# Optimization experiments

Hardware: AMD Instinct MI355X
Metric: run time of the kernel (lower is better)

The kernel has to match this reference:

```python
import jax, jax.numpy as jnp
import numpy as np

TOP_K = 2
TEMP = 1.0  # router_temperature


def setup_inputs() -> dict:
    key = jax.random.key(0)
    ks = jax.random.split(key, 6)
    B, L, D, F, E, DT = 32, 2048, 512, 1024, 8, 16
    x = jax.random.normal(ks[0], (B, L, D), dtype=jnp.float32)
    z_task = jax.random.normal(ks[1], (B, DT), dtype=jnp.float32)
    tau = jnp.ones((B, 1), dtype=jnp.float32)
    Wr = jax.random.normal(ks[2], (D + DT, E), dtype=jnp.float32) * 0.02
    br = jnp.zeros((E,), dtype=jnp.float32)
    W1 = jax.random.normal(ks[3], (E, D, F), dtype=jnp.float32) * 0.02
    b1 = jnp.zeros((E, F), dtype=jnp.float32)
    W2 = jax.random.normal(ks[4], (E, F, D), dtype=jnp.float32) * 0.02
    b2 = jnp.zeros((E, D), dtype=jnp.float32)
    return dict(x=x, z_task=z_task, tau=tau, Wr=Wr, br=br, W1=W1, b1=b1, W2=W2, b2=b2)


def reference(x, z_task, tau, Wr, br, W1, b1, W2, b2):
    """TaskAdaptiveMoE forward: task-conditioned top-k router + expert dispatch/combine.

    x: [B, L, D], z_task: [B, d_task], tau: [B, 1]. Returns (y [B,L,D], aux_loss scalar).
    """
    B, L, D = x.shape
    E = Wr.shape[1]
    # Router fusion mode 'concat': concat token features with broadcast task token.
    z = jnp.broadcast_to(z_task[:, None, :], (B, L, z_task.shape[-1]))
    router_in = jnp.concatenate([x, z], axis=-1)            # [B, L, D+DT]
    logits = router_in @ Wr + br                             # [B, L, E]
    logits = logits / (TEMP * tau[:, :, None])               # temperature + per-sample tau

    # Top-k gating: softmax over the selected logits only.
    top_vals, top_idx = jax.lax.top_k(logits, TOP_K)         # [B, L, k]
    gates = jax.nn.softmax(top_vals, axis=-1)                # [B, L, k]
    onehot = jax.nn.one_hot(top_idx, E, dtype=x.dtype)       # [B, L, k, E]
    dense_gates = jnp.einsum('blk,blke->ble', gates, onehot)  # [B, L, E], sparse (top-k) combine weights

    # Dispatch/combine: loop over the small fixed expert set to bound memory.
    y = jnp.zeros_like(x)
    for e in range(E):
        h = jax.nn.gelu(x @ W1[e] + b1[e], approximate=False)  # [B, L, F]
        y = y + dense_gates[..., e:e + 1] * (h @ W2[e] + b2[e])

    # Load-balancing auxiliary loss: E * sum(load_fraction * mean_router_prob).
    probs = jax.nn.softmax(logits, axis=-1)                  # [B, L, E]
    importance = probs.mean(axis=(0, 1))                     # [E]
    load = onehot.sum(axis=2).mean(axis=(0, 1))              # [E] fraction of tokens hitting expert
    aux_loss = E * jnp.sum(load * importance)
    return y, aux_loss
```

## Files before the change

kernel.cpp:

```cpp
#include <hip/hip_runtime.h>
#include <hip/hip_bf16.h>
#include <math.h>

typedef _Float16 f16;
typedef __attribute__((ext_vector_type(8))) _Float16 f16x8;
typedef __attribute__((ext_vector_type(4))) float f32x4;

#define TOKENS 65536
#define D_ 512
#define F_ 1024
#define E_ 8
#define DT_ 16
#define TEMP_ 1.0f
#define RANKBIT (1 << 30)

#define OFF_CNT   0
#define OFF_IMP   64
#define OFF_TOK   4096
#define OFF_GATE  (OFF_TOK  + E_*TOKENS*4)
#define OFF_W1P   (OFF_GATE + E_*TOKENS*4)
#define OFF_W2P   (OFF_W1P  + E_*F_*D_*2)
#define OFF_REC1  (OFF_W2P  + E_*F_*D_*2)
#define REC1_BYTES ((size_t)TOKENS * D_ * 2)
#define WS_NEED   ((size_t)OFF_REC1 + REC1_BYTES)

__global__ __launch_bounds__(256) void k_pack(const float* __restrict__ src,
                                              f16* __restrict__ dst, int R, int C)
{
  __shared__ float tile[128][17];
  int e = blockIdx.z, ct = blockIdx.y, kp = blockIdx.x;
  const float* s = src + (size_t)e * R * C + (size_t)(kp * 128) * C + ct * 16;
  int t = threadIdx.x;
  int c = t & 15, r0 = t >> 4;
  #pragma unroll
  for (int p = 0; p < 8; ++p)
    tile[r0 + p * 16][c] = s[(size_t)(r0 + p * 16) * C + c];
  __syncthreads();
  int ksl = t >> 6, l = t & 63, l15 = l & 15, lq = l >> 4;
  f16x8 v;
  #pragma unroll
  for (int j = 0; j < 8; ++j) v[j] = (f16)tile[ksl * 32 + lq * 8 + j][l15];
  f16* d = dst + ((((size_t)e * (C / 16) + ct) * (R / 32)) + kp * 4 + ksl) * 512 + l * 8;
  *(f16x8*)d = v;
}

__global__ __launch_bounds__(256) void k_router(
    const float* __restrict__ x, const float* __restrict__ z, const float* __restrict__ tau,
    const float* __restrict__ Wr, const float* __restrict__ br,
    int* __restrict__ gcnt, float* __restrict__ gimp,
    int* __restrict__ tokrec, float* __restrict__ gaterec)
{
  __shared__ float zlog[E_];
  __shared__ float stau;
  __shared__ int   recI[128];
  __shared__ float rg0[128], rg1[128];
  __shared__ int   pos0[128], pos1[128];
  __shared__ int   lcnt[E_], lbase[E_];
  __shared__ float limp[E_];

  int tid = threadIdx.x, lane = tid & 63, w = tid >> 6;
  int t0 = blockIdx.x * 128;
  int b = t0 >> 11;

  if (tid < E_) {
    float s = br[tid];
    #pragma unroll
    for (int dt = 0; dt < DT_; ++dt) s += z[b * DT_ + dt] * Wr[(D_ + dt) * E_ + tid];
    zlog[tid] = s;
    lcnt[tid] = 0; limp[tid] = 0.f;
  }
  if (tid == 0) stau = TEMP_ * tau[b];

  float wreg[8][8];
  const float* wp = Wr + lane * 64;
  #pragma unroll
  for (int j = 0; j < 8; ++j) {
    f32x4 a = *(const f32x4*)(wp + j * 8);
    f32x4 c = *(const f32x4*)(wp + j * 8 + 4);
    wreg[j][0]=a[0]; wreg[j][1]=a[1]; wreg[j][2]=a[2]; wreg[j][3]=a[3];
    wreg[j][4]=c[0]; wreg[j][5]=c[1]; wreg[j][6]=c[2]; wreg[j][7]=c[3];
  }
  __syncthreads();
  float tv = stau;
  float imp[E_];
  #pragma unroll
  for (int e2 = 0; e2 < E_; ++e2) imp[e2] = 0.f;

  for (int i = 0; i < 32; ++i) {
    int li = w * 32 + i;
    int t = t0 + li;
    const float* xr = x + (size_t)t * D_ + lane * 8;
    f32x4 xa = *(const f32x4*)xr;
    f32x4 xb = *(const f32x4*)(xr + 4);
    float v[E_];
    #pragma unroll
    for (int e2 = 0; e2 < E_; ++e2)
      v[e2] = xa[0]*wreg[0][e2] + xa[1]*wreg[1][e2] + xa[2]*wreg[2][e2] + xa[3]*wreg[3][e2]
            + xb[0]*wreg[4][e2] + xb[1]*wreg[5][e2] + xb[2]*wreg[6][e2] + xb[3]*wreg[7][e2];
    #pragma unroll
    for (int s = 0; s < 6; ++s) {
      #pragma unroll
      for (int e2 = 0; e2 < E_; ++e2) v[e2] += __shfl_xor(v[e2], 1 << s, 64);
    }
    if (lane == 0) {
      #pragma unroll
      for (int e2 = 0; e2 < E_; ++e2) v[e2] = (v[e2] + zlog[e2]) / tv;
      int i0 = 0; float b0v = v[0];
      #pragma unroll
      for (int e2 = 1; e2 < E_; ++e2) if (v[e2] > b0v) { b0v = v[e2]; i0 = e2; }
      int i1 = -1; float b1v = -3.4e38f;
      #pragma unroll
      for (int e2 = 0; e2 < E_; ++e2) if (e2 != i0 && v[e2] > b1v) { b1v = v[e2]; i1 = e2; }
      float ee = expf(b1v - b0v);
      float g0 = 1.f / (1.f + ee);
      recI[li] = i0 | (i1 << 4);
      rg0[li] = g0; rg1[li] = ee * g0;
      float ssum = 0.f, pe[E_];
      #pragma unroll
      for (int e2 = 0; e2 < E_; ++e2) { pe[e2] = expf(v[e2] - b0v); ssum += pe[e2]; }
      float inv = 1.f / ssum;
      #pragma unroll
      for (int e2 = 0; e2 < E_; ++e2) imp[e2] += pe[e2] * inv;
    }
  }
  if (lane == 0) {
    #pragma unroll
    for (int e2 = 0; e2 < E_; ++e2) atomicAdd(&limp[e2], imp[e2]);
  }
  __syncthreads();
  if (tid < 128) {
    int r = recI[tid], i0 = r & 15, i1 = r >> 4;
    pos0[tid] = atomicAdd(&lcnt[i0], 1);
    pos1[tid] = atomicAdd(&lcnt[i1], 1);
  }
  __syncthreads();
  if (tid < E_) {
    lbase[tid] = atomicAdd(&gcnt[tid], lcnt[tid]);
    atomicAdd(&gimp[tid], limp[tid]);
  }
  __syncthreads();
  if (tid < 128) {
    int r = recI[tid], i0 = r & 15, i1 = r >> 4;
    int t = t0 + tid;
    int o0 = i0 * TOKENS + lbase[i0] + pos0[tid];
    int o1 = i1 * TOKENS + lbase[i1] + pos1[tid];
    tokrec[o0] = t;            gaterec[o0] = rg0[tid];
    tokrec[o1] = t | RANKBIT;  gaterec[o1] = rg1[tid];
  }
}

__device__ __forceinline__ float gelu_f(float v)
{
  float u = v * 0.70710678118654752f;
  float au = fabsf(u);
  float t = __builtin_amdgcn_rcpf(1.f + 0.3275911f * au);
  float p = t * (0.254829592f + t * (-0.284496736f + t * (1.421413741f +
            t * (-1.453152027f + t * 1.061405429f))));
  float er = 1.f - p * __expf(-u * u);
  return 0.5f * v * (1.f + copysignf(er, v));
}

__global__ __launch_bounds__(1024, 4) void k_mlp(
    const float* __restrict__ x,
    const f16* __restrict__ W1p, const float* __restrict__ b1,
    const f16* __restrict__ W2p, const float* __restrict__ b2,
    const int* __restrict__ gcnt, const int* __restrict__ tokrec,
    const float* __restrict__ gaterec,
    f16* __restrict__ rec1, float* __restrict__ y, int use_rec)
{
  int e    = blockIdx.x & 7;
  int tile = blockIdx.x >> 3;
  int cnt  = gcnt[e];
  int start = tile * 128;
  if (start >= cnt) return;

  __shared__ f16   xs[128 * 512];
  __shared__ f16   hs[128 * 64];
  __shared__ int   stok[128];
  __shared__ float sgate[128];

  int tid = threadIdx.x, lane = tid & 63, w = tid >> 6;
  int l15 = lane & 15, lq = lane >> 4, lk8 = lq * 8;

  const int*   tokE  = tokrec  + e * TOKENS;
  const float* gateE = gaterec + e * TOKENS;

  if (tid < 128) {
    int idx = start + tid;
    stok[tid]  = (idx < cnt) ? tokE[idx]  : -1;
    sgate[tid] = (idx < cnt) ? gateE[idx] : 0.f;
  }
  __syncthreads();

  #pragma unroll
  for (int i = 0; i < 8; ++i) {
    int r = w * 8 + i;
    int trec = stok[r];
    f32x4 a = {0.f,0.f,0.f,0.f}, bv = {0.f,0.f,0.f,0.f};
    if (trec >= 0) {
      const float* p = x + (size_t)(trec & 0x3FFFFFFF) * D_ + lane * 8;
      a  = *(const f32x4*)p;
      bv = *(const f32x4*)(p + 4);
    }
    f16x8 pk;
    pk[0]=(f16)a[0];  pk[1]=(f16)a[1];  pk[2]=(f16)a[2];  pk[3]=(f16)a[3];
    pk[4]=(f16)bv[0]; pk[5]=(f16)bv[1]; pk[6]=(f16)bv[2]; pk[7]=(f16)bv[3];
    int off = (r * 1024 + lane * 16) ^ ((r & 7) << 4);
    *(f16x8*)((char*)xs + off) = pk;
  }
  __syncthreads();

  f32x4 yacc[4][4];
  #pragma unroll
  for (int mt = 0; mt < 4; ++mt)
    #pragma unroll
    for (int nt = 0; nt < 4; ++nt) {
      yacc[mt][nt][0]=0.f; yacc[mt][nt][1]=0.f; yacc[mt][nt][2]=0.f; yacc[mt][nt][3]=0.f;
    }

  int rga = w >> 2, cta = w & 3;
  int rgb = w >> 3, csb = w & 7;
  const f16* w1b = W1p + (size_t)e * (64 * 16 * 512);
  const f16* w2b = W2p + (size_t)e * (32 * 32 * 512);

  for (int it = 0; it < 16; ++it) {
    float b1v = b1[e * F_ + it * 64 + cta * 16 + l15];
    const f16* pA = w1b + ((size_t)(it * 4 + cta) * 16) * 512 + lane * 8;
    f32x4 h0 = {0.f,0.f,0.f,0.f}, h1 = {0.f,0.f,0.f,0.f};
    int r0b = rga * 32 + l15, r1b = r0b + 16;
    #pragma unroll
    for (int ks = 0; ks < 16; ++ks) {
      f16x8 wf = *(const f16x8*)(pA + (size_t)ks * 512);
      int k2 = (ks * 32 + lk8) * 2;
      f16x8 a0 = *(const f16x8*)((const char*)xs + ((r0b * 1024 + k2) ^ ((r0b & 7) << 4)));
      f16x8 a1 = *(const f16x8*)((const char*)xs + ((r1b * 1024 + k2) ^ ((r1b & 7) << 4)));
      h0 = __builtin_amdgcn_mfma_f32_16x16x32_f16(a0, wf, h0, 0, 0, 0);
      h1 = __builtin_amdgcn_mfma_f32_16x16x32_f16(a1, wf, h1, 0, 0, 0);
    }
    #pragma unroll
    for (int rg = 0; rg < 4; ++rg) {
      h0[rg] = gelu_f(h0[rg] + b1v);
      h1[rg] = gelu_f(h1[rg] + b1v);
    }
    __syncthreads();
    #pragma unroll
    for (int mt = 0; mt < 2; ++mt) {
      #pragma unroll
      for (int rg = 0; rg < 4; ++rg) {
        int row = rga * 32 + mt * 16 + lq * 4 + rg;
        int off = (row * 128 + (cta * 16 + l15) * 2) ^ ((row & 7) << 4);
        *(f16*)((char*)hs + off) = (f16)(mt ? h1[rg] : h0[rg]);
      }
    }
    __syncthreads();

    #pragma unroll
    for (int ks = 0; ks < 2; ++ks) {
      f16x8 wfB[4];
      #pragma unroll
      for (int nt = 0; nt < 4; ++nt)
        wfB[nt] = *(const f16x8*)(w2b + (((size_t)(csb * 4 + nt)) * 32 + it * 2 + ks) * 512 + lane * 8);
      f16x8 afr[4];
      #pragma unroll
      for (int mt = 0; mt < 4; ++mt) {
        int row = rgb * 64 + mt * 16 + l15;
        int off = (row * 128 + (ks * 32 + lk8) * 2) ^ ((row & 7) << 4);
        afr[mt] = *(const f16x8*)((const char*)hs + off);
      }
      #pragma unroll
      for (int nt = 0; nt < 4; ++nt)
        #pragma unroll
        for (int mt = 0; mt < 4; ++mt)
          yacc[mt][nt] = __builtin_amdgcn_mfma_f32_16x16x32_f16(afr[mt], wfB[nt], yacc[mt][nt], 0, 0, 0);
    }
  }

  float b2s[4];
  #pragma unroll
  for (int nt = 0; nt < 4; ++nt) b2s[nt] = b2[e * D_ + csb * 64 + nt * 16 + l15];

  if (use_rec) {
    #pragma unroll
    for (int mt = 0; mt < 4; ++mt) {
      #pragma unroll
      for (int rg = 0; rg < 4; ++rg) {
        int row = rgb * 64 + mt * 16 + lq * 4 + rg;
        float g = sgate[row];
        #pragma unroll
        for (int nt = 0; nt < 4; ++nt) {
          int col = csb * 64 + nt * 16 + l15;
          int off = (row * 1024 + col * 2) ^ ((row & 7) << 4);
          *(f16*)((char*)xs + off) = (f16)(g * (yacc[mt][nt][rg] + b2s[nt]));
        }
      }
    }
    __syncthreads();
    #pragma unroll
    for (int i = 0; i < 8; ++i) {
      int r = w * 8 + i;
      int trec = stok[r];
      if (trec < 0) continue;
      size_t tk = (size_t)(trec & 0x3FFFFFFF);
      f16x8 v = *(const f16x8*)((const char*)xs + ((r * 1024 + lane * 16) ^ ((r & 7) << 4)));
      if (trec & RANKBIT) {
        *(f16x8*)(rec1 + tk * D_ + lane * 8) = v;
      } else {
        f32x4 lo, hi;
        lo[0]=(float)v[0]; lo[1]=(float)v[1]; lo[2]=(float)v[2]; lo[3]=(float)v[3];
        hi[0]=(float)v[4]; hi[1]=(float)v[5]; hi[2]=(float)v[6]; hi[3]=(float)v[7];
        float* yp = y + tk * D_ + lane * 8;
        *(f32x4*)yp = lo;
        *(f32x4*)(yp + 4) = hi;
      }
    }
  } else {
    #pragma unroll
    for (int mt = 0; mt < 4; ++mt) {
      #pragma unroll
      for (int rg = 0; rg < 4; ++rg) {
        int row = rgb * 64 + mt * 16 + lq * 4 + rg;
        int trec = stok[row];
        if (trec < 0) continue;
        float g = sgate[row];
        size_t tk = (size_t)(trec & 0x3FFFFFFF);
        float* yp = y + tk * D_ + csb * 64 + l15;
        #pragma unroll
        for (int nt = 0; nt < 4; ++nt)
          atomicAdd(yp + nt * 16, g * (yacc[mt][nt][rg] + b2s[nt]));
      }
    }
  }
}

__global__ __launch_bounds__(256) void k_combine(const f16* __restrict__ rec1,
                                                 float* __restrict__ y)
{
  size_t i = (size_t)blockIdx.x * 256 + threadIdx.x;
  size_t n = (size_t)TOKENS * (D_ / 8);
  size_t stride = (size_t)gridDim.x * 256;
  for (; i < n; i += stride) {
    f16x8 r = *((const f16x8*)rec1 + i);
    float* yp = y + i * 8;
    f32x4 lo = *(const f32x4*)yp;
    f32x4 hi = *((const f32x4*)yp + 1);
    lo[0] += (float)r[0]; lo[1] += (float)r[1]; lo[2] += (float)r[2]; lo[3] += (float)r[3];
    hi[0] += (float)r[4]; hi[1] += (float)r[5]; hi[2] += (float)r[6]; hi[3] += (float)r[7];
    *(f32x4*)yp = lo;
    *((f32x4*)yp + 1) = hi;
  }
}

__global__ void k_aux(const int* __restrict__ gcnt, const float* __restrict__ gimp,
                      float* __restrict__ outp)
{
  if (threadIdx.x == 0) {
    float a = 0.f;
    for (int e2 = 0; e2 < E_; ++e2)
      a += ((float)gcnt[e2] * (1.f / 65536.f)) * (gimp[e2] * (1.f / 65536.f));
    outp[0] = (float)E_ * a;
  }
}

extern "C" void kernel_launch(void* const* d_in, const int* in_sizes, int n_in,
                              void* d_out, int out_size, void* d_ws, size_t ws_size,
                              hipStream_t stream)
{
  const float* x   = (const float*)d_in[0];
  const float* z   = (const float*)d_in[1];
  const float* tau = (const float*)d_in[2];
  const float* Wr  = (const float*)d_in[3];
  const float* br  = (const float*)d_in[4];
  const float* W1  = (const float*)d_in[5];
  const float* b1  = (const float*)d_in[6];
  const float* W2  = (const float*)d_in[7];
  const float* b2  = (const float*)d_in[8];
  float* out = (float*)d_out;
  char*  ws  = (char*)d_ws;

  int*   gcnt    = (int*)  (ws + OFF_CNT);
  float* gimp    = (float*)(ws + OFF_IMP);
  int*   tokrec  = (int*)  (ws + OFF_TOK);
  float* gaterec = (float*)(ws + OFF_GATE);
  f16*   W1p     = (f16*)  (ws + OFF_W1P);
  f16*   W2p     = (f16*)  (ws + OFF_W2P);
  f16*   rec1    = (f16*)  (ws + OFF_REC1);

  int use_rec = (ws_size >= WS_NEED) ? 1 : 0;

  hipMemsetAsync(ws, 0, 4096, stream);
  if (!use_rec)
    hipMemsetAsync(d_out, 0, (size_t)out_size * 4, stream);

  k_pack<<<dim3(D_/128, F_/16, E_), 256, 0, stream>>>(W1, W1p, D_, F_);
  k_pack<<<dim3(F_/128, D_/16, E_), 256, 0, stream>>>(W2, W2p, F_, D_);

  k_router<<<TOKENS / 128, 256, 0, stream>>>(x, z, tau, Wr, br, gcnt, gimp,
                                             tokrec, gaterec);

  k_mlp<<<E_ * (TOKENS / 128), 1024, 0, stream>>>(x, W1p, b1, W2p, b2, gcnt,
                                                  tokrec, gaterec, rec1, out, use_rec);

  if (use_rec)
    k_combine<<<2048, 256, 0, stream>>>(rec1, out);

  k_aux<<<1, 64, 0, stream>>>(gcnt, gimp, out + (size_t)TOKENS * D_);
}
```

Before: 924.5 us.

## Shrink MLP tiles to 64 tokens and software-pipeline the two GEMM stages

The expert MLP kernel now processes 64-token tiles with 512-thread blocks instead of 128 tokens with 1024 threads. The F dimension is walked in 128-wide chunks, and the first GEMM plus GELU for the next chunk is issued before the second GEMM of the current chunk, so the two stages can overlap. Token and gate shared-memory staging is replaced by per-thread register copies and direct global reads. The smaller tile lowers LDS use and may raise occupancy, but each W1/W2 weight fragment is reused across half as many tokens, which increases weight traffic, and the extra live accumulators raise register pressure.

```diff
diff --git a/kernel.cpp b/kernel.cpp
--- a/kernel.cpp
+++ b/kernel.cpp
@@ -160,7 +160,7 @@
   return 0.5f * v * (1.f + copysignf(er, v));
 }
 
-__global__ __launch_bounds__(1024, 4) void k_mlp(
+__global__ __launch_bounds__(512, 4) void k_mlp(
     const float* __restrict__ x,
     const f16* __restrict__ W1p, const float* __restrict__ b1,
     const f16* __restrict__ W2p, const float* __restrict__ b2,
@@ -171,13 +171,11 @@
   int e    = blockIdx.x & 7;
   int tile = blockIdx.x >> 3;
   int cnt  = gcnt[e];
-  int start = tile * 128;
+  int start = tile * 64;
   if (start >= cnt) return;
 
-  __shared__ f16   xs[128 * 512];
-  __shared__ f16   hs[128 * 64];
-  __shared__ int   stok[128];
-  __shared__ float sgate[128];
+  __shared__ f16 xs[64 * 512];
+  __shared__ f16 hs[64 * 128];
 
   int tid = threadIdx.x, lane = tid & 63, w = tid >> 6;
   int l15 = lane & 15, lq = lane >> 4, lk8 = lq * 8;
@@ -185,20 +183,19 @@
   const int*   tokE  = tokrec  + e * TOKENS;
   const float* gateE = gaterec + e * TOKENS;
 
-  if (tid < 128) {
-    int idx = start + tid;
-    stok[tid]  = (idx < cnt) ? tokE[idx]  : -1;
-    sgate[tid] = (idx < cnt) ? gateE[idx] : 0.f;
-  }
-  __syncthreads();
+  int tok[8];
+  #pragma unroll
+  for (int i = 0; i < 8; ++i) {
+    int idx = start + w * 8 + i;
+    tok[i] = (idx < cnt) ? tokE[idx] : -1;
+  }
 
   #pragma unroll
   for (int i = 0; i < 8; ++i) {
     int r = w * 8 + i;
-    int trec = stok[r];
     f32x4 a = {0.f,0.f,0.f,0.f}, bv = {0.f,0.f,0.f,0.f};
-    if (trec >= 0) {
-      const float* p = x + (size_t)(trec & 0x3FFFFFFF) * D_ + lane * 8;
+    if (tok[i] >= 0) {
+      const float* p = x + (size_t)(tok[i] & 0x3FFFFFFF) * D_ + lane * 8;
       a  = *(const f32x4*)p;
       bv = *(const f32x4*)(p + 4);
     }
@@ -218,60 +215,86 @@
       yacc[mt][nt][0]=0.f; yacc[mt][nt][1]=0.f; yacc[mt][nt][2]=0.f; yacc[mt][nt][3]=0.f;
     }
 
-  int rga = w >> 2, cta = w & 3;
-  int rgb = w >> 3, csb = w & 7;
+  int rga = w >> 2;
+  int cta = w & 3;
+  int csb = w;
   const f16* w1b = W1p + (size_t)e * (64 * 16 * 512);
   const f16* w2b = W2p + (size_t)e * (32 * 32 * 512);
 
-  for (int it = 0; it < 16; ++it) {
-    float b1v = b1[e * F_ + it * 64 + cta * 16 + l15];
-    const f16* pA = w1b + ((size_t)(it * 4 + cta) * 16) * 512 + lane * 8;
-    f32x4 h0 = {0.f,0.f,0.f,0.f}, h1 = {0.f,0.f,0.f,0.f};
-    int r0b = rga * 32 + l15, r1b = r0b + 16;
-    #pragma unroll
-    for (int ks = 0; ks < 16; ++ks) {
-      f16x8 wf = *(const f16x8*)(pA + (size_t)ks * 512);
-      int k2 = (ks * 32 + lk8) * 2;
-      f16x8 a0 = *(const f16x8*)((const char*)xs + ((r0b * 1024 + k2) ^ ((r0b & 7) << 4)));
-      f16x8 a1 = *(const f16x8*)((const char*)xs + ((r1b * 1024 + k2) ^ ((r1b & 7) << 4)));
-      h0 = __builtin_amdgcn_mfma_f32_16x16x32_f16(a0, wf, h0, 0, 0, 0);
-      h1 = __builtin_amdgcn_mfma_f32_16x16x32_f16(a1, wf, h1, 0, 0, 0);
-    }
-    #pragma unroll
-    for (int rg = 0; rg < 4; ++rg) {
-      h0[rg] = gelu_f(h0[rg] + b1v);
-      h1[rg] = gelu_f(h1[rg] + b1v);
-    }
+  int r0b = rga * 32 + l15, r1b = r0b + 16;
+
+  f32x4 hA[2][2];
+  float b1v[2];
+  #define STAGE_A(ITV)                                                          \
+  {                                                                             \
+    int c0 = (ITV) * 8 + cta * 2;                                               \
+    b1v[0] = b1[e * F_ + c0 * 16 + l15];                                        \
+    b1v[1] = b1[e * F_ + (c0 + 1) * 16 + l15];                                  \
+    const f16* p0 = w1b + ((size_t)c0 * 16) * 512 + lane * 8;                   \
+    const f16* p1 = p0 + 16 * 512;                                              \
+    _Pragma("unroll")                                                           \
+    for (int rt = 0; rt < 2; ++rt)                                              \
+      _Pragma("unroll")                                                         \
+      for (int ct = 0; ct < 2; ++ct) {                                          \
+        hA[rt][ct][0]=0.f; hA[rt][ct][1]=0.f; hA[rt][ct][2]=0.f; hA[rt][ct][3]=0.f; \
+      }                                                                         \
+    _Pragma("unroll")                                                           \
+    for (int ks = 0; ks < 16; ++ks) {                                           \
+      f16x8 wf0 = *(const f16x8*)(p0 + (size_t)ks * 512);                       \
+      f16x8 wf1 = *(const f16x8*)(p1 + (size_t)ks * 512);                       \
+      int k2 = (ks * 32 + lk8) * 2;                                             \
+      f16x8 a0 = *(const f16x8*)((const char*)xs + ((r0b * 1024 + k2) ^ ((r0b & 7) << 4))); \
+      f16x8 a1 = *(const f16x8*)((const char*)xs + ((r1b * 1024 + k2) ^ ((r1b & 7) << 4))); \
+      hA[0][0] = __builtin_amdgcn_mfma_f32_16x16x32_f16(a0, wf0, hA[0][0], 0, 0, 0); \
+      hA[1][0] = __builtin_amdgcn_mfma_f32_16x16x32_f16(a1, wf0, hA[1][0], 0, 0, 0); \
+      hA[0][1] = __builtin_amdgcn_mfma_f32_16x16x32_f16(a0, wf1, hA[0][1], 0, 0, 0); \
+      hA[1][1] = __builtin_amdgcn_mfma_f32_16x16x32_f16(a1, wf1, hA[1][1], 0, 0, 0); \
+    }                                                                           \
+    _Pragma("unroll")                                                           \
+    for (int rt = 0; rt < 2; ++rt)                                              \
+      _Pragma("unroll")                                                         \
+      for (int ct = 0; ct < 2; ++ct)                                            \
+        _Pragma("unroll")                                                       \
+        for (int rg = 0; rg < 4; ++rg)                                          \
+          hA[rt][ct][rg] = gelu_f(hA[rt][ct][rg] + b1v[ct]);                    \
+  }
+
+  STAGE_A(0);
+
+  for (int it = 0; it < 8; ++it) {
     __syncthreads();
     #pragma unroll
-    for (int mt = 0; mt < 2; ++mt) {
-      #pragma unroll
-      for (int rg = 0; rg < 4; ++rg) {
-        int row = rga * 32 + mt * 16 + lq * 4 + rg;
-        int off = (row * 128 + (cta * 16 + l15) * 2) ^ ((row & 7) << 4);
-        *(f16*)((char*)hs + off) = (f16)(mt ? h1[rg] : h0[rg]);
-      }
-    }
+    for (int rt = 0; rt < 2; ++rt)
+      #pragma unroll
+      for (int ct = 0; ct < 2; ++ct)
+        #pragma unroll
+        for (int rg = 0; rg < 4; ++rg) {
+          int row = rga * 32 + rt * 16 + lq * 4 + rg;
+          int col = cta * 32 + ct * 16 + l15;
+          int off = (row * 256 + col * 2) ^ ((row & 7) << 4);
+          *(f16*)((char*)hs + off) = (f16)hA[rt][ct][rg];
+        }
     __syncthreads();
 
-    #pragma unroll
-    for (int ks = 0; ks < 2; ++ks) {
-      f16x8 wfB[4];
-      #pragma unroll
-      for (int nt = 0; nt < 4; ++nt)
-        wfB[nt] = *(const f16x8*)(w2b + (((size_t)(csb * 4 + nt)) * 32 + it * 2 + ks) * 512 + lane * 8);
+    if (it < 7) STAGE_A(it + 1);
+
+    #pragma unroll
+    for (int ks = 0; ks < 4; ++ks) {
+      int kglob = it * 4 + ks;
       f16x8 afr[4];
       #pragma unroll
       for (int mt = 0; mt < 4; ++mt) {
-        int row = rgb * 64 + mt * 16 + l15;
-        int off = (row * 128 + (ks * 32 + lk8) * 2) ^ ((row & 7) << 4);
+        int row = mt * 16 + l15;
+        int off = (row * 256 + (ks * 32 + lk8) * 2) ^ ((row & 7) << 4);
         afr[mt] = *(const f16x8*)((const char*)hs + off);
       }
       #pragma unroll
-      for (int nt = 0; nt < 4; ++nt)
+      for (int nt = 0; nt < 4; ++nt) {
+        f16x8 wfB = *(const f16x8*)(w2b + (((size_t)(csb * 4 + nt)) * 32 + kglob) * 512 + lane * 8);
         #pragma unroll
         for (int mt = 0; mt < 4; ++mt)
-          yacc[mt][nt] = __builtin_amdgcn_mfma_f32_16x16x32_f16(afr[mt], wfB[nt], yacc[mt][nt], 0, 0, 0);
+          yacc[mt][nt] = __builtin_amdgcn_mfma_f32_16x16x32_f16(afr[mt], wfB, yacc[mt][nt], 0, 0, 0);
+      }
     }
   }
 
@@ -284,8 +307,8 @@
     for (int mt = 0; mt < 4; ++mt) {
       #pragma unroll
       for (int rg = 0; rg < 4; ++rg) {
-        int row = rgb * 64 + mt * 16 + lq * 4 + rg;
-        float g = sgate[row];
+        int row = mt * 16 + lq * 4 + rg;
+        float g = (start + row < cnt) ? gateE[start + row] : 0.f;
         #pragma unroll
         for (int nt = 0; nt < 4; ++nt) {
           int col = csb * 64 + nt * 16 + l15;
@@ -298,7 +321,7 @@
     #pragma unroll
     for (int i = 0; i < 8; ++i) {
       int r = w * 8 + i;
-      int trec = stok[r];
+      int trec = tok[i];
       if (trec < 0) continue;
       size_t tk = (size_t)(trec & 0x3FFFFFFF);
       f16x8 v = *(const f16x8*)((const char*)xs + ((r * 1024 + lane * 16) ^ ((r & 7) << 4)));
@@ -318,15 +341,17 @@
     for (int mt = 0; mt < 4; ++mt) {
       #pragma unroll
       for (int rg = 0; rg < 4; ++rg) {
-        int row = rgb * 64 + mt * 16 + lq * 4 + rg;
-        int trec = stok[row];
-        if (trec < 0) continue;
-        float g = sgate[row];
-        size_t tk = (size_t)(trec & 0x3FFFFFFF);
-        float* yp = y + tk * D_ + csb * 64 + l15;
-        #pragma unroll
-        for (int nt = 0; nt < 4; ++nt)
-          atomicAdd(yp + nt * 16, g * (yacc[mt][nt][rg] + b2s[nt]));
+        int row = mt * 16 + lq * 4 + rg;
+        int ridx = start + row;
+        if (ridx < cnt) {
+          int trec = tokE[ridx];
+          float g  = gateE[ridx];
+          size_t tk = (size_t)(trec & 0x3FFFFFFF);
+          float* yp = y + tk * D_ + csb * 64 + l15;
+          #pragma unroll
+          for (int nt = 0; nt < 4; ++nt)
+            atomicAdd(yp + nt * 16, g * (yacc[mt][nt][rg] + b2s[nt]));
+        }
       }
     }
   }
@@ -397,8 +422,8 @@
   k_router<<<TOKENS / 128, 256, 0, stream>>>(x, z, tau, Wr, br, gcnt, gimp,
                                              tokrec, gaterec);
 
-  k_mlp<<<E_ * (TOKENS / 128), 1024, 0, stream>>>(x, W1p, b1, W2p, b2, gcnt,
-                                                  tokrec, gaterec, rec1, out, use_rec);
+  k_mlp<<<E_ * (TOKENS / 64), 512, 0, stream>>>(x, W1p, b1, W2p, b2, gcnt,
+                                                tokrec, gaterec, rec1, out, use_rec);
 
   if (use_rec)
     k_combine<<<2048, 256, 0, stream>>>(rec1, out);
```

After: 1.357 ms. +46.8%, slower.

## Widen per-warp GEMM1 tile to 32x32 and halve F-chunk iterations in expert MLP

Applied to the files above, without the earlier changes.

Each warp now computes two 16-column F tiles per iteration, so every xs A-fragment read from LDS feeds two MFMAs. The F-chunk loop drops from 16 to 8 iterations of 128 columns, and the hs handoff is split into two 64-column halves. The first W2 fragments are prefetched before the barrier, and the token/gate shared-memory staging is replaced by per-thread registers and direct global reads. The aim is to cut LDS traffic and barriers per FLOP and hide W2 load latency, at the cost of more registers, duplicated gate/token global loads, and idle warps during each hs write phase.

```diff
diff --git a/kernel.cpp b/kernel.cpp
--- a/kernel.cpp
+++ b/kernel.cpp
@@ -174,10 +174,8 @@
   int start = tile * 128;
   if (start >= cnt) return;
 
-  __shared__ f16   xs[128 * 512];
-  __shared__ f16   hs[128 * 64];
-  __shared__ int   stok[128];
-  __shared__ float sgate[128];
+  __shared__ f16 xs[128 * 512];
+  __shared__ f16 hs[128 * 64];
 
   int tid = threadIdx.x, lane = tid & 63, w = tid >> 6;
   int l15 = lane & 15, lq = lane >> 4, lk8 = lq * 8;
@@ -185,20 +183,19 @@
   const int*   tokE  = tokrec  + e * TOKENS;
   const float* gateE = gaterec + e * TOKENS;
 
-  if (tid < 128) {
-    int idx = start + tid;
-    stok[tid]  = (idx < cnt) ? tokE[idx]  : -1;
-    sgate[tid] = (idx < cnt) ? gateE[idx] : 0.f;
-  }
-  __syncthreads();
+  int tok[8];
+  #pragma unroll
+  for (int i = 0; i < 8; ++i) {
+    int idx = start + w * 8 + i;
+    tok[i] = (idx < cnt) ? tokE[idx] : -1;
+  }
 
   #pragma unroll
   for (int i = 0; i < 8; ++i) {
     int r = w * 8 + i;
-    int trec = stok[r];
     f32x4 a = {0.f,0.f,0.f,0.f}, bv = {0.f,0.f,0.f,0.f};
-    if (trec >= 0) {
-      const float* p = x + (size_t)(trec & 0x3FFFFFFF) * D_ + lane * 8;
+    if (tok[i] >= 0) {
+      const float* p = x + (size_t)(tok[i] & 0x3FFFFFFF) * D_ + lane * 8;
       a  = *(const f32x4*)p;
       bv = *(const f32x4*)(p + 4);
     }
@@ -218,60 +215,90 @@
       yacc[mt][nt][0]=0.f; yacc[mt][nt][1]=0.f; yacc[mt][nt][2]=0.f; yacc[mt][nt][3]=0.f;
     }
 
-  int rga = w >> 2, cta = w & 3;
+  int rga = w >> 2, cpa = w & 3;
   int rgb = w >> 3, csb = w & 7;
   const f16* w1b = W1p + (size_t)e * (64 * 16 * 512);
   const f16* w2b = W2p + (size_t)e * (32 * 32 * 512);
-
-  for (int it = 0; it < 16; ++it) {
-    float b1v = b1[e * F_ + it * 64 + cta * 16 + l15];
-    const f16* pA = w1b + ((size_t)(it * 4 + cta) * 16) * 512 + lane * 8;
-    f32x4 h0 = {0.f,0.f,0.f,0.f}, h1 = {0.f,0.f,0.f,0.f};
-    int r0b = rga * 32 + l15, r1b = r0b + 16;
+  int r0b = rga * 32 + l15, r1b = r0b + 16;
+
+  for (int it = 0; it < 8; ++it) {
+    int c0 = it * 8 + cpa * 2;
+    float b1v0 = b1[e * F_ + c0 * 16 + l15];
+    float b1v1 = b1[e * F_ + (c0 + 1) * 16 + l15];
+    const f16* p0 = w1b + ((size_t)c0 * 16) * 512 + lane * 8;
+    const f16* p1 = p0 + 16 * 512;
+    f32x4 hA[2][2];
+    #pragma unroll
+    for (int rt = 0; rt < 2; ++rt)
+      #pragma unroll
+      for (int ct = 0; ct < 2; ++ct) {
+        hA[rt][ct][0]=0.f; hA[rt][ct][1]=0.f; hA[rt][ct][2]=0.f; hA[rt][ct][3]=0.f;
+      }
     #pragma unroll
     for (int ks = 0; ks < 16; ++ks) {
-      f16x8 wf = *(const f16x8*)(pA + (size_t)ks * 512);
+      f16x8 wf0 = *(const f16x8*)(p0 + (size_t)ks * 512);
+      f16x8 wf1 = *(const f16x8*)(p1 + (size_t)ks * 512);
       int k2 = (ks * 32 + lk8) * 2;
       f16x8 a0 = *(const f16x8*)((const char*)xs + ((r0b * 1024 + k2) ^ ((r0b & 7) << 4)));
       f16x8 a1 = *(const f16x8*)((const char*)xs + ((r1b * 1024 + k2) ^ ((r1b & 7) << 4)));
-      h0 = __builtin_amdgcn_mfma_f32_16x16x32_f16(a0, wf, h0, 0, 0, 0);
-      h1 = __builtin_amdgcn_mfma_f32_16x16x32_f16(a1, wf, h1, 0, 0, 0);
-    }
-    #pragma unroll
-    for (int rg = 0; rg < 4; ++rg) {
-      h0[rg] = gelu_f(h0[rg] + b1v);
-      h1[rg] = gelu_f(h1[rg] + b1v);
-    }
-    __syncthreads();
-    #pragma unroll
-    for (int mt = 0; mt < 2; ++mt) {
+      hA[0][0] = __builtin_amdgcn_mfma_f32_16x16x32_f16(a0, wf0, hA[0][0], 0, 0, 0);
+      hA[1][0] = __builtin_amdgcn_mfma_f32_16x16x32_f16(a1, wf0, hA[1][0], 0, 0, 0);
+      hA[0][1] = __builtin_amdgcn_mfma_f32_16x16x32_f16(a0, wf1, hA[0][1], 0, 0, 0);
+      hA[1][1] = __builtin_amdgcn_mfma_f32_16x16x32_f16(a1, wf1, hA[1][1], 0, 0, 0);
+    }
+    #pragma unroll
+    for (int rt = 0; rt < 2; ++rt)
       #pragma unroll
       for (int rg = 0; rg < 4; ++rg) {
-        int row = rga * 32 + mt * 16 + lq * 4 + rg;
-        int off = (row * 128 + (cta * 16 + l15) * 2) ^ ((row & 7) << 4);
-        *(f16*)((char*)hs + off) = (f16)(mt ? h1[rg] : h0[rg]);
-      }
-    }
-    __syncthreads();
-
-    #pragma unroll
-    for (int ks = 0; ks < 2; ++ks) {
-      f16x8 wfB[4];
+        hA[rt][0][rg] = gelu_f(hA[rt][0][rg] + b1v0);
+        hA[rt][1][rg] = gelu_f(hA[rt][1][rg] + b1v1);
+      }
+
+    #pragma unroll
+    for (int h = 0; h < 2; ++h) {
+      f16x8 pre[4];
       #pragma unroll
       for (int nt = 0; nt < 4; ++nt)
-        wfB[nt] = *(const f16x8*)(w2b + (((size_t)(csb * 4 + nt)) * 32 + it * 2 + ks) * 512 + lane * 8);
-      f16x8 afr[4];
-      #pragma unroll
-      for (int mt = 0; mt < 4; ++mt) {
-        int row = rgb * 64 + mt * 16 + l15;
-        int off = (row * 128 + (ks * 32 + lk8) * 2) ^ ((row & 7) << 4);
-        afr[mt] = *(const f16x8*)((const char*)hs + off);
-      }
-      #pragma unroll
-      for (int nt = 0; nt < 4; ++nt)
+        pre[nt] = *(const f16x8*)(w2b + (((size_t)(csb * 4 + nt)) * 32 + it * 4 + h * 2) * 512 + lane * 8);
+      __syncthreads();
+      if ((cpa >> 1) == h) {
         #pragma unroll
-        for (int mt = 0; mt < 4; ++mt)
-          yacc[mt][nt] = __builtin_amdgcn_mfma_f32_16x16x32_f16(afr[mt], wfB[nt], yacc[mt][nt], 0, 0, 0);
+        for (int rt = 0; rt < 2; ++rt)
+          #pragma unroll
+          for (int ct = 0; ct < 2; ++ct)
+            #pragma unroll
+            for (int rg = 0; rg < 4; ++rg) {
+              int row = rga * 32 + rt * 16 + lq * 4 + rg;
+              int col = (cpa & 1) * 32 + ct * 16 + l15;
+              int off = (row * 128 + col * 2) ^ ((row & 7) << 4);
+              *(f16*)((char*)hs + off) = (f16)hA[rt][ct][rg];
+            }
+      }
+      __syncthreads();
+      #pragma unroll
+      for (int ks = 0; ks < 2; ++ks) {
+        f16x8 wfB[4];
+        if (ks == 0) {
+          #pragma unroll
+          for (int nt = 0; nt < 4; ++nt) wfB[nt] = pre[nt];
+        } else {
+          #pragma unroll
+          for (int nt = 0; nt < 4; ++nt)
+            wfB[nt] = *(const f16x8*)(w2b + (((size_t)(csb * 4 + nt)) * 32 + it * 4 + h * 2 + 1) * 512 + lane * 8);
+        }
+        f16x8 afr[4];
+        #pragma unroll
+        for (int mt = 0; mt < 4; ++mt) {
+          int row = rgb * 64 + mt * 16 + l15;
+          int off = (row * 128 + (ks * 32 + lk8) * 2) ^ ((row & 7) << 4);
+          afr[mt] = *(const f16x8*)((const char*)hs + off);
+        }
+        #pragma unroll
+        for (int nt = 0; nt < 4; ++nt)
+          #pragma unroll
+          for (int mt = 0; mt < 4; ++mt)
+            yacc[mt][nt] = __builtin_amdgcn_mfma_f32_16x16x32_f16(afr[mt], wfB[nt], yacc[mt][nt], 0, 0, 0);
+      }
     }
   }
 
@@ -285,7 +312,7 @@
       #pragma unroll
       for (int rg = 0; rg < 4; ++rg) {
         int row = rgb * 64 + mt * 16 + lq * 4 + rg;
-        float g = sgate[row];
+        float g = (start + row < cnt) ? gateE[start + row] : 0.f;
         #pragma unroll
         for (int nt = 0; nt < 4; ++nt) {
           int col = csb * 64 + nt * 16 + l15;
@@ -298,7 +325,7 @@
     #pragma unroll
     for (int i = 0; i < 8; ++i) {
       int r = w * 8 + i;
-      int trec = stok[r];
+      int trec = tok[i];
       if (trec < 0) continue;
       size_t tk = (size_t)(trec & 0x3FFFFFFF);
       f16x8 v = *(const f16x8*)((const char*)xs + ((r * 1024 + lane * 16) ^ ((r & 7) << 4)));
@@ -319,14 +346,16 @@
       #pragma unroll
       for (int rg = 0; rg < 4; ++rg) {
         int row = rgb * 64 + mt * 16 + lq * 4 + rg;
-        int trec = stok[row];
-        if (trec < 0) continue;
-        float g = sgate[row];
-        size_t tk = (size_t)(trec & 0x3FFFFFFF);
-        float* yp = y + tk * D_ + csb * 64 + l15;
-        #pragma unroll
-        for (int nt = 0; nt < 4; ++nt)
-          atomicAdd(yp + nt * 16, g * (yacc[mt][nt][rg] + b2s[nt]));
+        int ridx = start + row;
+        if (ridx < cnt) {
+          int trec = tokE[ridx];
+          float g  = gateE[ridx];
+          size_t tk = (size_t)(trec & 0x3FFFFFFF);
+          float* yp = y + tk * D_ + csb * 64 + l15;
+          #pragma unroll
+          for (int nt = 0; nt < 4; ++nt)
+            atomicAdd(yp + nt * 16, g * (yacc[mt][nt][rg] + b2s[nt]));
+        }
       }
     }
   }
```

Result: slower. 1.503 ms (+62.6%).
